# Optimization experiments

Hardware: AMD Instinct MI355X
Metric: run time of the kernel (lower is better)

Reference implementation:

```python
import jax, jax.numpy as jnp
import numpy as np

B, N, E = 8, 4096, 65536
FIN, OUT, T, H = 128, 128, 4, 4
C = OUT // H  # per-head channels
NEG_SLOPE = 0.2
EPS_LN = 1e-5


def setup_inputs() -> dict:
    key = jax.random.key(0)
    ks = jax.random.split(key, 10)
    x = jax.random.normal(ks[0], (B, N, FIN), dtype=jnp.float32)
    edge_index = jax.random.randint(ks[1], (B, 2, E), 0, N, dtype=jnp.int64)
    edge_type = jax.random.randint(ks[2], (B, E), 0, T, dtype=jnp.int64)
    # per-edge-type GATConv params (PyG GATConv: lin weight, att_src, att_dst, bias)
    W = jax.random.normal(ks[3], (T, FIN, H * C), dtype=jnp.float32) / np.sqrt(FIN)
    a_src = jax.random.normal(ks[4], (T, H, C), dtype=jnp.float32) / np.sqrt(C)
    a_dst = jax.random.normal(ks[5], (T, H, C), dtype=jnp.float32) / np.sqrt(C)
    bias = jnp.zeros((T, H * C), dtype=jnp.float32)
    gamma = jnp.ones((OUT,), dtype=jnp.float32)
    beta = jnp.zeros((OUT,), dtype=jnp.float32)
    return {"x": x, "edge_index": edge_index, "edge_type": edge_type,
            "W": W, "a_src": a_src, "a_dst": a_dst, "bias": bias,
            "gamma": gamma, "beta": beta}


def _gat_aggregate(h, src, dst, mask):
    """Single-graph masked GAT aggregation.
    h: [N,H,C] transformed features; src,dst: [E]; mask: [E] bool.
    Returns [N,H,C].
    """
    n = h.shape[0]
    a_s = h[src]                     # [E,H,C] source features (messages)
    # attention logits: att_src . h_src + att_dst . h_dst, done by caller via h-dot
    return a_s, n


def reference(x, edge_index, edge_type, W, a_src, a_dst, bias, gamma, beta):
    b, n, _ = x.shape
    src = edge_index[:, 0, :]  # [B,E]
    dst = edge_index[:, 1, :]

    def per_graph(e_logit, src_b, dst_b, mask_b, h_b):
        # e_logit: [E,H]; h_b: [N,H,C]
        e_m = jnp.where(mask_b[:, None], e_logit, -1e30)
        m = jax.ops.segment_max(e_m, dst_b, num_segments=n)      # [N,H]
        m = jnp.maximum(m, -1e30)
        ex = jnp.exp(e_m - m[dst_b]) * mask_b[:, None]           # [E,H]
        den = jax.ops.segment_sum(ex, dst_b, num_segments=n)     # [N,H]
        alpha = ex / (den[dst_b] + 1e-16)                        # [E,H]
        msg = alpha[:, :, None] * h_b[src_b]                     # [E,H,C]
        return jax.ops.segment_sum(msg, dst_b, num_segments=n)   # [N,H,C]

    out = jnp.zeros((b, n, H * C), dtype=x.dtype)
    for t in range(T):
        h = jnp.einsum('bnf,fo->bno', x, W[t]).reshape(b, n, H, C)
        al_s = jnp.einsum('bnhc,hc->bnh', h, a_src[t])           # [B,N,H]
        al_d = jnp.einsum('bnhc,hc->bnh', h, a_dst[t])
        e = jax.nn.leaky_relu(
            jnp.take_along_axis(al_s, src[..., None], axis=1) +
            jnp.take_along_axis(al_d, dst[..., None], axis=1),
            negative_slope=NEG_SLOPE)                            # [B,E,H]
        mask = (edge_type == t)
        agg = jax.vmap(per_graph)(e, src, dst, mask, h)          # [B,N,H,C]
        out = out + agg.reshape(b, n, H * C) + bias[t]
    # residual + LayerNorm (dropout is identity in eval)
    y = x + out
    mu = jnp.mean(y, axis=-1, keepdims=True)
    var = jnp.var(y, axis=-1, keepdims=True)
    return (y - mu) / jnp.sqrt(var + EPS_LN) * gamma + beta
```

## Files before the change

### kernel.cpp

```cpp
#include <hip/hip_runtime.h>

typedef unsigned int uint;
typedef unsigned short ushort;
typedef __attribute__((ext_vector_type(8))) short short8;
typedef __attribute__((ext_vector_type(4))) float f32x4;

#define Bb 8
#define Nn 4096
#define Ee 65536
#define Tt 4

__device__ __forceinline__ ushort bf16_rne_u(float f) {
    uint u = __float_as_uint(f);
    u += 0x7FFFu + ((u >> 16) & 1u);
    return (ushort)(u >> 16);
}

__global__ __launch_bounds__(256) void prepack_w_kernel(
    const float* __restrict__ W, ushort* __restrict__ Wf)
{
    int gid = blockIdx.x * 256 + threadIdx.x;
    int t    = gid >> 11;
    int rem  = gid & 2047;
    int ks   = rem >> 9;
    int rem2 = rem & 511;
    int nt   = rem2 >> 6;
    int lane = rem2 & 63;
    int n  = nt * 16 + (lane & 15);
    int g  = lane >> 4;
    int k0 = ks * 32 + 4 * g;

    const float* Wt = W + t * 16384;
    union { uint4 q; ushort u[8]; } P;
#pragma unroll
    for (int j = 0; j < 4; ++j) P.u[j]     = bf16_rne_u(Wt[(size_t)(k0 + j) * 128 + n]);
#pragma unroll
    for (int j = 0; j < 4; ++j) P.u[4 + j] = bf16_rne_u(Wt[(size_t)(k0 + 16 + j) * 128 + n]);
    *reinterpret_cast<uint4*>(Wf + (size_t)gid * 8) = P.q;
}

__global__ __launch_bounds__(256, 4) void gemm_mfma_kernel(
    const float* __restrict__ x, const ushort* __restrict__ Wf,
    const float* __restrict__ a_src, const float* __restrict__ a_dst,
    ushort* __restrict__ h, float* __restrict__ al_s, float* __restrict__ al_d)
{
    __shared__ ushort Wlds[16384];
    __shared__ ushort Hst[4096];

    int blk    = blockIdx.x;
    int b      = blk >> 7;
    int rowblk = blk & 127;
    int tid  = threadIdx.x;
    int w    = tid >> 6;
    int lane = tid & 63;
    int nl = lane & 15;
    int g  = lane >> 4;
    int rg  = w & 1;
    int chn = w >> 1;
    int row0 = rowblk * 32 + rg * 16;

    short8 Ah[4], Al[4];
    {
        const float* xr = x + ((size_t)b * Nn + row0 + nl) * 128;
#pragma unroll
        for (int ks = 0; ks < 4; ++ks) {
            float4 fa = *reinterpret_cast<const float4*>(xr + ks * 32 + 4 * g);
            float4 fb = *reinterpret_cast<const float4*>(xr + ks * 32 + 16 + 4 * g);
            float v[8] = {fa.x, fa.y, fa.z, fa.w, fb.x, fb.y, fb.z, fb.w};
            union { short8 s; ushort u[8]; } H, L;
#pragma unroll
            for (int j = 0; j < 8; ++j) {
                ushort hi = bf16_rne_u(v[j]);
                float fh = __uint_as_float(((uint)hi) << 16);
                H.u[j] = hi;
                L.u[j] = bf16_rne_u(v[j] - fh);
            }
            Ah[ks] = H.s;
            Al[ks] = L.s;
        }
    }

    for (int t = 0; t < Tt; ++t) {
        {
            const uint4* src = reinterpret_cast<const uint4*>(Wf + (size_t)t * 16384);
#pragma unroll
            for (int i = 0; i < 8; ++i) {
                uint4 v = src[i * 256 + tid];
                *reinterpret_cast<uint4*>(&Wlds[(i * 256 + tid) * 8]) = v;
            }
        }
        __syncthreads();

        f32x4 acc[4];
#pragma unroll
        for (int i = 0; i < 4; ++i) acc[i] = (f32x4){0.f, 0.f, 0.f, 0.f};
#pragma unroll
        for (int ks = 0; ks < 4; ++ks) {
#pragma unroll
            for (int i = 0; i < 4; ++i) {
                int ntg = chn * 4 + i;
                union { uint4 q; short8 s; } F;
                F.q = *reinterpret_cast<const uint4*>(&Wlds[((ks * 8 + ntg) * 64 + lane) * 8]);
                acc[i] = __builtin_amdgcn_mfma_f32_16x16x32_bf16(Ah[ks], F.s, acc[i], 0, 0, 0);
                acc[i] = __builtin_amdgcn_mfma_f32_16x16x32_bf16(Al[ks], F.s, acc[i], 0, 0, 0);
            }
        }

        {
            float as[4], ad[4];
#pragma unroll
            for (int i = 0; i < 4; ++i) {
                as[i] = a_src[t * 128 + chn * 64 + i * 16 + nl];
                ad[i] = a_dst[t * 128 + chn * 64 + i * 16 + nl];
            }
#pragma unroll
            for (int ih = 0; ih < 2; ++ih) {
#pragma unroll
                for (int r = 0; r < 4; ++r) {
                    float ps = acc[2 * ih][r] * as[2 * ih] + acc[2 * ih + 1][r] * as[2 * ih + 1];
                    float pd = acc[2 * ih][r] * ad[2 * ih] + acc[2 * ih + 1][r] * ad[2 * ih + 1];
#pragma unroll
                    for (int off = 1; off < 16; off <<= 1) {
                        ps += __shfl_xor(ps, off);
                        pd += __shfl_xor(pd, off);
                    }
                    if (nl == 0) {
                        int rowg = row0 + 4 * g + r;
                        int head = 2 * chn + ih;
                        al_s[((size_t)(b * Tt + t) * Nn + rowg) * 4 + head] = ps;
                        al_d[((size_t)(b * Tt + t) * Nn + rowg) * 4 + head] = pd;
                    }
                }
            }
        }

#pragma unroll
        for (int i = 0; i < 4; ++i) {
#pragma unroll
            for (int r = 0; r < 4; ++r) {
                int rowl = rg * 16 + 4 * g + r;
                int col  = chn * 64 + i * 16 + nl;
                uint e = (uint)(rowl * 128) + ((uint)col ^ (uint)(((rowl >> 2) & 3) << 3));
                Hst[e] = bf16_rne_u(acc[i][r]);
            }
        }
        __syncthreads();

        {
            ushort* hb = h + ((size_t)(b * Tt + t) * Nn + (size_t)rowblk * 32) * 128;
#pragma unroll
            for (int it = 0; it < 2; ++it) {
                uint f = (uint)(it * 2048 + tid * 8);
                int rowl = f >> 7;
                uint e = (f & ~127u) + ((f & 127u) ^ (uint)(((rowl >> 2) & 3) << 3));
                uint4 v = *reinterpret_cast<const uint4*>(&Hst[e]);
                *reinterpret_cast<uint4*>(hb + f) = v;
            }
        }
    }
}

__global__ __launch_bounds__(256) void count_kernel(
    const int* __restrict__ ei, const int* __restrict__ et, uint* __restrict__ count)
{
    int i = blockIdx.x * 256 + threadIdx.x;
    int b = i >> 16;
    int e = i & (Ee - 1);
    int dst = ei[(size_t)b * 2 * Ee + Ee + e];
    int t = et[(size_t)b * Ee + e];
    atomicAdd(&count[(((uint)(b * Nn + dst)) << 2) | (uint)t], 1u);
}

__global__ __launch_bounds__(256) void scan1_kernel(
    const uint* __restrict__ cnt, uint* __restrict__ offs, uint* __restrict__ bsum)
{
    __shared__ uint ws[4];
    int tid = threadIdx.x, lane = tid & 63, wv = tid >> 6;
    uint4 c = reinterpret_cast<const uint4*>(cnt)[blockIdx.x * 256 + tid];
    uint tot = c.x + c.y + c.z + c.w;
    uint inc = tot;
#pragma unroll
    for (int d = 1; d < 64; d <<= 1) {
        uint tv = (uint)__shfl_up((int)inc, d);
        if (lane >= d) inc += tv;
    }
    if (lane == 63) ws[wv] = inc;
    __syncthreads();
    uint wexcl = 0;
    for (int w = 0; w < wv; ++w) wexcl += ws[w];
    uint P = wexcl + inc - tot;
    uint4 o;
    o.x = P; o.y = P + c.x; o.z = o.y + c.y; o.w = o.z + c.z;
    reinterpret_cast<uint4*>(offs)[blockIdx.x * 256 + tid] = o;
    if (tid == 255) bsum[blockIdx.x] = P + tot;
}

__global__ __launch_bounds__(128) void scan2_kernel(
    const uint* __restrict__ bsum, uint* __restrict__ bsx)
{
    __shared__ uint w0tot;
    int tid = threadIdx.x, lane = tid & 63, wv = tid >> 6;
    uint v = bsum[tid], inc = v;
#pragma unroll
    for (int d = 1; d < 64; d <<= 1) {
        uint tv = (uint)__shfl_up((int)inc, d);
        if (lane >= d) inc += tv;
    }
    if (tid == 63) w0tot = inc;
    __syncthreads();
    uint add = (wv == 1) ? w0tot : 0u;
    bsx[tid] = add + inc - v;
}

__global__ __launch_bounds__(256) void scatter_lr_kernel(
    const int* __restrict__ ei, const int* __restrict__ et,
    const float* __restrict__ al_s, const float* __restrict__ al_d,
    const uint* __restrict__ offs, const uint* __restrict__ bsx,
    uint* __restrict__ cursor, uint* __restrict__ src_sorted, float4* __restrict__ lr_sorted)
{
    int i = blockIdx.x * 256 + threadIdx.x;
    int b = i >> 16;
    int e = i & (Ee - 1);
    int src = ei[(size_t)b * 2 * Ee + e];
    int dst = ei[(size_t)b * 2 * Ee + Ee + e];
    int t = et[(size_t)b * Ee + e];
    uint g = (((uint)(b * Nn + dst)) << 2) | (uint)t;
    uint slot = atomicAdd(&cursor[g], 1u);
    uint p = offs[g] + bsx[g >> 10] + slot;

    size_t btN = (size_t)(b * Tt + t) * Nn;
    float4 s4 = *reinterpret_cast<const float4*>(&al_s[(btN + src) * 4]);
    float4 d4 = *reinterpret_cast<const float4*>(&al_d[(btN + dst) * 4]);
    float4 lr;
    lr.x = s4.x + d4.x; lr.x = lr.x > 0.f ? lr.x : 0.2f * lr.x;
    lr.y = s4.y + d4.y; lr.y = lr.y > 0.f ? lr.y : 0.2f * lr.y;
    lr.z = s4.z + d4.z; lr.z = lr.z > 0.f ? lr.z : 0.2f * lr.z;
    lr.w = s4.w + d4.w; lr.w = lr.w > 0.f ? lr.w : 0.2f * lr.w;
    src_sorted[p] = (uint)src;
    lr_sorted[p] = lr;
}

__global__ __launch_bounds__(256) void gat_ln_kernel(
    const float* __restrict__ x, const ushort* __restrict__ h,
    const uint* __restrict__ count, const uint* __restrict__ offs, const uint* __restrict__ bsx,
    const uint* __restrict__ src_sorted, const float4* __restrict__ lr_sorted,
    const float* __restrict__ bias, const float* __restrict__ gamma, const float* __restrict__ beta,
    float* __restrict__ out)
{
    __shared__ uint  su_s[4][128];
    __shared__ float ew_s[4][512];
    int wl = threadIdx.x >> 6;
    uint*  su = su_s[wl];
    float* ew = ew_s[wl];

    int wid  = blockIdx.x * 4 + wl;
    int lane = threadIdx.x & 63;
    int b   = wid >> 12;
    int dst = wid & (Nn - 1);
    int eg = lane >> 4;
    int cl = lane & 15;
    int c0 = cl << 3;
    int hh = cl >> 2;

    uint4 cnt4 = reinterpret_cast<const uint4*>(count)[wid];
    uint4 off4 = reinterpret_cast<const uint4*>(offs)[wid];
    uint bsxv  = bsx[((uint)wid) >> 8];
    uint base  = off4.x + bsxv;
    uint D     = min(off4.w + cnt4.w - off4.x, 128u);

    for (uint i = lane; i < D; i += 64) {
        float4 l4 = lr_sorted[base + i];
        su[i] = src_sorted[base + i];
        ew[i * 4 + 0] = __expf(l4.x);
        ew[i * 4 + 1] = __expf(l4.y);
        ew[i * 4 + 2] = __expf(l4.z);
        ew[i * 4 + 3] = __expf(l4.w);
    }

    uint rel[4];
    rel[0] = 0;
    rel[1] = off4.y - off4.x;
    rel[2] = off4.z - off4.x;
    rel[3] = off4.w - off4.x;
    uint ctv[4] = {cnt4.x, cnt4.y, cnt4.z, cnt4.w};

    float tot[8];
#pragma unroll
    for (int k = 0; k < 8; ++k) tot[k] = 0.f;

    for (int t = 0; t < Tt; ++t) {
        uint ct = ctv[t];
        if (!ct) continue;
        uint p0 = rel[t];
        const ushort* hs = h + (size_t)(b * Tt + t) * Nn * 128;

        float acc[8];
#pragma unroll
        for (int k = 0; k < 8; ++k) acc[k] = 0.f;
        float denacc = 0.f;

        for (uint j = 0; j < ct; j += 4) {
            uint jj = j + (uint)eg;
            bool valid = jj < ct;
            uint idx = min(p0 + jj, 127u);
            uint sj = su[idx] & 4095u;
            float aw = valid ? ew[idx * 4 + hh] : 0.f;
            uint4 hv = *reinterpret_cast<const uint4*>(hs + (size_t)sj * 128 + c0);
            float f0 = __uint_as_float(hv.x << 16);
            float f1 = __uint_as_float(hv.x & 0xFFFF0000u);
            float f2 = __uint_as_float(hv.y << 16);
            float f3 = __uint_as_float(hv.y & 0xFFFF0000u);
            float f4 = __uint_as_float(hv.z << 16);
            float f5 = __uint_as_float(hv.z & 0xFFFF0000u);
            float f6 = __uint_as_float(hv.w << 16);
            float f7 = __uint_as_float(hv.w & 0xFFFF0000u);
            acc[0] += aw * f0; acc[1] += aw * f1;
            acc[2] += aw * f2; acc[3] += aw * f3;
            acc[4] += aw * f4; acc[5] += aw * f5;
            acc[6] += aw * f6; acc[7] += aw * f7;
            denacc += aw;
        }
        float d = denacc;
        d += __shfl_xor(d, 1); d += __shfl_xor(d, 2);
        d += __shfl_xor(d, 16); d += __shfl_xor(d, 32);
        float rden = 4.f / (d + 4e-16f);
#pragma unroll
        for (int k = 0; k < 8; ++k) tot[k] += acc[k] * rden;
    }

#pragma unroll
    for (int k = 0; k < 8; ++k) {
        tot[k] += __shfl_xor(tot[k], 16);
        tot[k] += __shfl_xor(tot[k], 32);
    }

    size_t obase = ((size_t)b * Nn + dst) * 128 + c0;
    float y[8];
    {
        float4 xa = *reinterpret_cast<const float4*>(x + obase);
        float4 xb = *reinterpret_cast<const float4*>(x + obase + 4);
        float bs[8];
#pragma unroll
        for (int k = 0; k < 8; ++k) bs[k] = 0.f;
#pragma unroll
        for (int t = 0; t < Tt; ++t) {
            float4 ba = *reinterpret_cast<const float4*>(bias + t * 128 + c0);
            float4 bb = *reinterpret_cast<const float4*>(bias + t * 128 + c0 + 4);
            bs[0] += ba.x; bs[1] += ba.y; bs[2] += ba.z; bs[3] += ba.w;
            bs[4] += bb.x; bs[5] += bb.y; bs[6] += bb.z; bs[7] += bb.w;
        }
        y[0] = xa.x + tot[0] + bs[0]; y[1] = xa.y + tot[1] + bs[1];
        y[2] = xa.z + tot[2] + bs[2]; y[3] = xa.w + tot[3] + bs[3];
        y[4] = xb.x + tot[4] + bs[4]; y[5] = xb.y + tot[5] + bs[5];
        y[6] = xb.z + tot[6] + bs[6]; y[7] = xb.w + tot[7] + bs[7];
    }

    float s = 0.f, ss = 0.f;
#pragma unroll
    for (int k = 0; k < 8; ++k) { s += y[k]; ss += y[k] * y[k]; }
#pragma unroll
    for (int off = 1; off < 16; off <<= 1) {
        s += __shfl_xor(s, off);
        ss += __shfl_xor(ss, off);
    }
    float mu = s * (1.f / 128.f);
    float var = ss * (1.f / 128.f) - mu * mu;
    float rstd = rsqrtf(var + 1e-5f);

    if (eg == 0) {
        float4 ga = *reinterpret_cast<const float4*>(gamma + c0);
        float4 gb = *reinterpret_cast<const float4*>(gamma + c0 + 4);
        float4 ea = *reinterpret_cast<const float4*>(beta + c0);
        float4 eb = *reinterpret_cast<const float4*>(beta + c0 + 4);
        float4 o1, o2;
        o1.x = (y[0] - mu) * rstd * ga.x + ea.x;
        o1.y = (y[1] - mu) * rstd * ga.y + ea.y;
        o1.z = (y[2] - mu) * rstd * ga.z + ea.z;
        o1.w = (y[3] - mu) * rstd * ga.w + ea.w;
        o2.x = (y[4] - mu) * rstd * gb.x + eb.x;
        o2.y = (y[5] - mu) * rstd * gb.y + eb.y;
        o2.z = (y[6] - mu) * rstd * gb.z + eb.z;
        o2.w = (y[7] - mu) * rstd * gb.w + eb.w;
        *reinterpret_cast<float4*>(out + obase) = o1;
        *reinterpret_cast<float4*>(out + obase + 4) = o2;
    }
}

extern "C" void kernel_launch(void* const* d_in, const int* in_sizes, int n_in,
                              void* d_out, int out_size, void* d_ws, size_t ws_size,
                              hipStream_t stream)
{
    const float* x     = (const float*)d_in[0];
    const int*   ei    = (const int*)d_in[1];
    const int*   et    = (const int*)d_in[2];
    const float* W     = (const float*)d_in[3];
    const float* a_src = (const float*)d_in[4];
    const float* a_dst = (const float*)d_in[5];
    const float* bias  = (const float*)d_in[6];
    const float* gamma = (const float*)d_in[7];
    const float* beta  = (const float*)d_in[8];
    float* out = (float*)d_out;

    ushort* h   = (ushort*)d_ws;
    size_t hsz  = (size_t)Bb * Tt * Nn * 128;
    float* al_s = (float*)(h + hsz);
    size_t alsz = (size_t)Bb * Tt * Nn * 4;
    float* al_d = al_s + alsz;
    uint* count  = (uint*)(al_d + alsz);
    uint* cursor = count + (size_t)Bb * Tt * Nn;
    uint* offs   = cursor + (size_t)Bb * Tt * Nn;
    uint* bsum   = offs + (size_t)Bb * Tt * Nn;
    uint* bsx    = bsum + 128;
    uint* src_sorted = bsx + 128;
    float4* lr_sorted = (float4*)(src_sorted + (size_t)Bb * Ee);
    ushort* Wf = (ushort*)(lr_sorted + (size_t)Bb * Ee);

    hipMemsetAsync(count, 0, (size_t)Bb * Tt * Nn * 2 * sizeof(uint), stream);

    prepack_w_kernel<<<32, 256, 0, stream>>>(W, Wf);
    gemm_mfma_kernel<<<Bb * 128, 256, 0, stream>>>(x, Wf, a_src, a_dst, h, al_s, al_d);

    count_kernel<<<(Bb * Ee) / 256, 256, 0, stream>>>(ei, et, count);
    scan1_kernel<<<128, 256, 0, stream>>>(count, offs, bsum);
    scan2_kernel<<<1, 128, 0, stream>>>(bsum, bsx);
    scatter_lr_kernel<<<(Bb * Ee) / 256, 256, 0, stream>>>(
        ei, et, al_s, al_d, offs, bsx, cursor, src_sorted, lr_sorted);

    gat_ln_kernel<<<(Bb * Nn) / 4, 256, 0, stream>>>(
        x, h, count, offs, bsx, src_sorted, lr_sorted, bias, gamma, beta, out);
}
```

Baseline: 206.1 us.

## Fuse preprocessing kernels and remap GAT aggregation to 16-lane groups per node

Merges the count and W-prepack kernels into one launch that also precomputes the summed bias, and folds scan1 into the GEMM launch as extra blocks. The aggregation kernel now handles 16 destination nodes per block, one 16-lane group each, processing edges serially instead of splitting them across four lane groups. This removes the cross-lane shuffle reductions and cuts launch count. The risks are that per-group serial edge loops lengthen the dependency chain on high-degree nodes, and that the per-node edge cache shrinks from 128 to 96 entries.

```diff
diff --git a/kernel.cpp b/kernel.cpp
--- a/kernel.cpp
+++ b/kernel.cpp
@@ -16,41 +16,82 @@
     return (ushort)(u >> 16);
 }
 
-__global__ __launch_bounds__(256) void prepack_w_kernel(
-    const float* __restrict__ W, ushort* __restrict__ Wf)
-{
-    int gid = blockIdx.x * 256 + threadIdx.x;
-    int t    = gid >> 11;
-    int rem  = gid & 2047;
-    int ks   = rem >> 9;
-    int rem2 = rem & 511;
-    int nt   = rem2 >> 6;
-    int lane = rem2 & 63;
-    int n  = nt * 16 + (lane & 15);
-    int g  = lane >> 4;
-    int k0 = ks * 32 + 4 * g;
-
-    const float* Wt = W + t * 16384;
-    union { uint4 q; ushort u[8]; } P;
-#pragma unroll
-    for (int j = 0; j < 4; ++j) P.u[j]     = bf16_rne_u(Wt[(size_t)(k0 + j) * 128 + n]);
-#pragma unroll
-    for (int j = 0; j < 4; ++j) P.u[4 + j] = bf16_rne_u(Wt[(size_t)(k0 + 16 + j) * 128 + n]);
-    *reinterpret_cast<uint4*>(Wf + (size_t)gid * 8) = P.q;
-}
-
-__global__ __launch_bounds__(256, 4) void gemm_mfma_kernel(
+__global__ __launch_bounds__(256) void fused_a_kernel(
+    const int* __restrict__ ei, const int* __restrict__ et, uint* __restrict__ count,
+    const float* __restrict__ W, ushort* __restrict__ Wf,
+    const float* __restrict__ bias, float* __restrict__ bias_sum)
+{
+    int bid = blockIdx.x;
+    int tid = threadIdx.x;
+    if (bid < 2048) {
+        int i = bid * 256 + tid;
+        int b = i >> 16;
+        int e = i & (Ee - 1);
+        int dst = ei[(size_t)b * 2 * Ee + Ee + e];
+        int t = et[(size_t)b * Ee + e];
+        atomicAdd(&count[(((uint)(b * Nn + dst)) << 2) | (uint)t], 1u);
+    } else if (bid < 2080) {
+        int gid = (bid - 2048) * 256 + tid;
+        int t    = gid >> 11;
+        int rem  = gid & 2047;
+        int ks   = rem >> 9;
+        int rem2 = rem & 511;
+        int nt   = rem2 >> 6;
+        int lane = rem2 & 63;
+        int n  = nt * 16 + (lane & 15);
+        int g  = lane >> 4;
+        int k0 = ks * 32 + 4 * g;
+        const float* Wt = W + t * 16384;
+        union { uint4 q; ushort u[8]; } P;
+#pragma unroll
+        for (int j = 0; j < 4; ++j) P.u[j]     = bf16_rne_u(Wt[(size_t)(k0 + j) * 128 + n]);
+#pragma unroll
+        for (int j = 0; j < 4; ++j) P.u[4 + j] = bf16_rne_u(Wt[(size_t)(k0 + 16 + j) * 128 + n]);
+        *reinterpret_cast<uint4*>(Wf + (size_t)gid * 8) = P.q;
+    } else {
+        if (tid < 128)
+            bias_sum[tid] = bias[tid] + bias[128 + tid] + bias[256 + tid] + bias[384 + tid];
+    }
+}
+
+__global__ __launch_bounds__(256, 4) void fused_b_kernel(
     const float* __restrict__ x, const ushort* __restrict__ Wf,
     const float* __restrict__ a_src, const float* __restrict__ a_dst,
-    ushort* __restrict__ h, float* __restrict__ al_s, float* __restrict__ al_d)
+    ushort* __restrict__ h, float* __restrict__ al_s, float* __restrict__ al_d,
+    const uint* __restrict__ cnt, uint* __restrict__ offs, uint* __restrict__ bsum)
 {
     __shared__ ushort Wlds[16384];
     __shared__ ushort Hst[4096];
+
+    int tid = threadIdx.x;
+
+    if (blockIdx.x >= 1024) {
+        uint* ws = reinterpret_cast<uint*>(Hst);
+        int cblk = blockIdx.x - 1024;
+        int lane = tid & 63, wv = tid >> 6;
+        uint4 c = reinterpret_cast<const uint4*>(cnt)[cblk * 256 + tid];
+        uint tot = c.x + c.y + c.z + c.w;
+        uint inc = tot;
+#pragma unroll
+        for (int d = 1; d < 64; d <<= 1) {
+            uint tv = (uint)__shfl_up((int)inc, d);
+            if (lane >= d) inc += tv;
+        }
+        if (lane == 63) ws[wv] = inc;
+        __syncthreads();
+        uint wexcl = 0;
+        for (int w = 0; w < wv; ++w) wexcl += ws[w];
+        uint P = wexcl + inc - tot;
+        uint4 o;
+        o.x = P; o.y = P + c.x; o.z = o.y + c.y; o.w = o.z + c.z;
+        reinterpret_cast<uint4*>(offs)[cblk * 256 + tid] = o;
+        if (tid == 255) bsum[cblk] = P + tot;
+        return;
+    }
 
     int blk    = blockIdx.x;
     int b      = blk >> 7;
     int rowblk = blk & 127;
-    int tid  = threadIdx.x;
     int w    = tid >> 6;
     int lane = tid & 63;
     int nl = lane & 15;
@@ -160,41 +201,6 @@
     }
 }
 
-__global__ __launch_bounds__(256) void count_kernel(
-    const int* __restrict__ ei, const int* __restrict__ et, uint* __restrict__ count)
-{
-    int i = blockIdx.x * 256 + threadIdx.x;
-    int b = i >> 16;
-    int e = i & (Ee - 1);
-    int dst = ei[(size_t)b * 2 * Ee + Ee + e];
-    int t = et[(size_t)b * Ee + e];
-    atomicAdd(&count[(((uint)(b * Nn + dst)) << 2) | (uint)t], 1u);
-}
-
-__global__ __launch_bounds__(256) void scan1_kernel(
-    const uint* __restrict__ cnt, uint* __restrict__ offs, uint* __restrict__ bsum)
-{
-    __shared__ uint ws[4];
-    int tid = threadIdx.x, lane = tid & 63, wv = tid >> 6;
-    uint4 c = reinterpret_cast<const uint4*>(cnt)[blockIdx.x * 256 + tid];
-    uint tot = c.x + c.y + c.z + c.w;
-    uint inc = tot;
-#pragma unroll
-    for (int d = 1; d < 64; d <<= 1) {
-        uint tv = (uint)__shfl_up((int)inc, d);
-        if (lane >= d) inc += tv;
-    }
-    if (lane == 63) ws[wv] = inc;
-    __syncthreads();
-    uint wexcl = 0;
-    for (int w = 0; w < wv; ++w) wexcl += ws[w];
-    uint P = wexcl + inc - tot;
-    uint4 o;
-    o.x = P; o.y = P + c.x; o.z = o.y + c.y; o.w = o.z + c.z;
-    reinterpret_cast<uint4*>(offs)[blockIdx.x * 256 + tid] = o;
-    if (tid == 255) bsum[blockIdx.x] = P + tot;
-}
-
 __global__ __launch_bounds__(128) void scan2_kernel(
     const uint* __restrict__ bsum, uint* __restrict__ bsx)
 {
@@ -244,31 +250,33 @@
     const float* __restrict__ x, const ushort* __restrict__ h,
     const uint* __restrict__ count, const uint* __restrict__ offs, const uint* __restrict__ bsx,
     const uint* __restrict__ src_sorted, const float4* __restrict__ lr_sorted,
-    const float* __restrict__ bias, const float* __restrict__ gamma, const float* __restrict__ beta,
+    const float* __restrict__ bias_sum, const float* __restrict__ gamma, const float* __restrict__ beta,
     float* __restrict__ out)
 {
-    __shared__ uint  su_s[4][128];
-    __shared__ float ew_s[4][512];
-    int wl = threadIdx.x >> 6;
-    uint*  su = su_s[wl];
-    float* ew = ew_s[wl];
-
-    int wid  = blockIdx.x * 4 + wl;
-    int lane = threadIdx.x & 63;
-    int b   = wid >> 12;
-    int dst = wid & (Nn - 1);
-    int eg = lane >> 4;
+    __shared__ uint  su_s[16][96];
+    __shared__ float ew_s[16][96 * 4];
+
+    int tid = threadIdx.x;
+    int wl   = tid >> 6;
+    int lane = tid & 63;
+    int ng = lane >> 4;
     int cl = lane & 15;
     int c0 = cl << 3;
     int hh = cl >> 2;
+    int grp = wl * 4 + ng;
+    uint*  su = su_s[grp];
+    float* ew = ew_s[grp];
+
+    int wid = blockIdx.x * 16 + grp;
+    int b   = wid >> 12;
+    int dst = wid & (Nn - 1);
 
     uint4 cnt4 = reinterpret_cast<const uint4*>(count)[wid];
     uint4 off4 = reinterpret_cast<const uint4*>(offs)[wid];
-    uint bsxv  = bsx[((uint)wid) >> 8];
-    uint base  = off4.x + bsxv;
-    uint D     = min(off4.w + cnt4.w - off4.x, 128u);
-
-    for (uint i = lane; i < D; i += 64) {
+    uint base  = off4.x + bsx[((uint)wid) >> 8];
+    uint D     = min(off4.w + cnt4.w - off4.x, 96u);
+
+    for (uint i = cl; i < D; i += 16) {
         float4 l4 = lr_sorted[base + i];
         su[i] = src_sorted[base + i];
         ew[i * 4 + 0] = __expf(l4.x);
@@ -276,18 +284,16 @@
         ew[i * 4 + 2] = __expf(l4.z);
         ew[i * 4 + 3] = __expf(l4.w);
     }
-
-    uint rel[4];
-    rel[0] = 0;
-    rel[1] = off4.y - off4.x;
-    rel[2] = off4.z - off4.x;
-    rel[3] = off4.w - off4.x;
+    __syncthreads();
+
+    uint rel[4] = {0u, off4.y - off4.x, off4.z - off4.x, off4.w - off4.x};
     uint ctv[4] = {cnt4.x, cnt4.y, cnt4.z, cnt4.w};
 
     float tot[8];
 #pragma unroll
     for (int k = 0; k < 8; ++k) tot[k] = 0.f;
 
+#pragma unroll
     for (int t = 0; t < Tt; ++t) {
         uint ct = ctv[t];
         if (!ct) continue;
@@ -297,14 +303,12 @@
         float acc[8];
 #pragma unroll
         for (int k = 0; k < 8; ++k) acc[k] = 0.f;
-        float denacc = 0.f;
-
-        for (uint j = 0; j < ct; j += 4) {
-            uint jj = j + (uint)eg;
-            bool valid = jj < ct;
-            uint idx = min(p0 + jj, 127u);
-            uint sj = su[idx] & 4095u;
-            float aw = valid ? ew[idx * 4 + hh] : 0.f;
+        float den = 0.f;
+
+        for (uint j = 0; j < ct; ++j) {
+            uint i = p0 + j;
+            float aw = ew[i * 4 + hh];
+            uint  sj = su[i];
             uint4 hv = *reinterpret_cast<const uint4*>(hs + (size_t)sj * 128 + c0);
             float f0 = __uint_as_float(hv.x << 16);
             float f1 = __uint_as_float(hv.x & 0xFFFF0000u);
@@ -318,20 +322,11 @@
             acc[2] += aw * f2; acc[3] += aw * f3;
             acc[4] += aw * f4; acc[5] += aw * f5;
             acc[6] += aw * f6; acc[7] += aw * f7;
-            denacc += aw;
-        }
-        float d = denacc;
-        d += __shfl_xor(d, 1); d += __shfl_xor(d, 2);
-        d += __shfl_xor(d, 16); d += __shfl_xor(d, 32);
-        float rden = 4.f / (d + 4e-16f);
+            den += aw;
+        }
+        float rden = 1.f / (den + 1e-16f);
 #pragma unroll
         for (int k = 0; k < 8; ++k) tot[k] += acc[k] * rden;
-    }
-
-#pragma unroll
-    for (int k = 0; k < 8; ++k) {
-        tot[k] += __shfl_xor(tot[k], 16);
-        tot[k] += __shfl_xor(tot[k], 32);
     }
 
     size_t obase = ((size_t)b * Nn + dst) * 128 + c0;
@@ -339,20 +334,12 @@
     {
         float4 xa = *reinterpret_cast<const float4*>(x + obase);
         float4 xb = *reinterpret_cast<const float4*>(x + obase + 4);
-        float bs[8];
-#pragma unroll
-        for (int k = 0; k < 8; ++k) bs[k] = 0.f;
-#pragma unroll
-        for (int t = 0; t < Tt; ++t) {
-            float4 ba = *reinterpret_cast<const float4*>(bias + t * 128 + c0);
-            float4 bb = *reinterpret_cast<const float4*>(bias + t * 128 + c0 + 4);
-            bs[0] += ba.x; bs[1] += ba.y; bs[2] += ba.z; bs[3] += ba.w;
-            bs[4] += bb.x; bs[5] += bb.y; bs[6] += bb.z; bs[7] += bb.w;
-        }
-        y[0] = xa.x + tot[0] + bs[0]; y[1] = xa.y + tot[1] + bs[1];
-        y[2] = xa.z + tot[2] + bs[2]; y[3] = xa.w + tot[3] + bs[3];
-        y[4] = xb.x + tot[4] + bs[4]; y[5] = xb.y + tot[5] + bs[5];
-        y[6] = xb.z + tot[6] + bs[6]; y[7] = xb.w + tot[7] + bs[7];
+        float4 ba = *reinterpret_cast<const float4*>(bias_sum + c0);
+        float4 bb = *reinterpret_cast<const float4*>(bias_sum + c0 + 4);
+        y[0] = xa.x + tot[0] + ba.x; y[1] = xa.y + tot[1] + ba.y;
+        y[2] = xa.z + tot[2] + ba.z; y[3] = xa.w + tot[3] + ba.w;
+        y[4] = xb.x + tot[4] + bb.x; y[5] = xb.y + tot[5] + bb.y;
+        y[6] = xb.z + tot[6] + bb.z; y[7] = xb.w + tot[7] + bb.w;
     }
 
     float s = 0.f, ss = 0.f;
@@ -367,23 +354,21 @@
     float var = ss * (1.f / 128.f) - mu * mu;
     float rstd = rsqrtf(var + 1e-5f);
 
-    if (eg == 0) {
-        float4 ga = *reinterpret_cast<const float4*>(gamma + c0);
-        float4 gb = *reinterpret_cast<const float4*>(gamma + c0 + 4);
-        float4 ea = *reinterpret_cast<const float4*>(beta + c0);
-        float4 eb = *reinterpret_cast<const float4*>(beta + c0 + 4);
-        float4 o1, o2;
-        o1.x = (y[0] - mu) * rstd * ga.x + ea.x;
-        o1.y = (y[1] - mu) * rstd * ga.y + ea.y;
-        o1.z = (y[2] - mu) * rstd * ga.z + ea.z;
-        o1.w = (y[3] - mu) * rstd * ga.w + ea.w;
-        o2.x = (y[4] - mu) * rstd * gb.x + eb.x;
-        o2.y = (y[5] - mu) * rstd * gb.y + eb.y;
-        o2.z = (y[6] - mu) * rstd * gb.z + eb.z;
-        o2.w = (y[7] - mu) * rstd * gb.w + eb.w;
-        *reinterpret_cast<float4*>(out + obase) = o1;
-        *reinterpret_cast<float4*>(out + obase + 4) = o2;
-    }
+    float4 ga = *reinterpret_cast<const float4*>(gamma + c0);
+    float4 gb = *reinterpret_cast<const float4*>(gamma + c0 + 4);
+    float4 ea = *reinterpret_cast<const float4*>(beta + c0);
+    float4 eb = *reinterpret_cast<const float4*>(beta + c0 + 4);
+    float4 o1, o2;
+    o1.x = (y[0] - mu) * rstd * ga.x + ea.x;
+    o1.y = (y[1] - mu) * rstd * ga.y + ea.y;
+    o1.z = (y[2] - mu) * rstd * ga.z + ea.z;
+    o1.w = (y[3] - mu) * rstd * ga.w + ea.w;
+    o2.x = (y[4] - mu) * rstd * gb.x + eb.x;
+    o2.y = (y[5] - mu) * rstd * gb.y + eb.y;
+    o2.z = (y[6] - mu) * rstd * gb.z + eb.z;
+    o2.w = (y[7] - mu) * rstd * gb.w + eb.w;
+    *reinterpret_cast<float4*>(out + obase) = o1;
+    *reinterpret_cast<float4*>(out + obase + 4) = o2;
 }
 
 extern "C" void kernel_launch(void* const* d_in, const int* in_sizes, int n_in,
@@ -411,21 +396,19 @@
     uint* offs   = cursor + (size_t)Bb * Tt * Nn;
     uint* bsum   = offs + (size_t)Bb * Tt * Nn;
     uint* bsx    = bsum + 128;
-    uint* src_sorted = bsx + 128;
+    float* bias_sum = (float*)(bsx + 128);
+    uint* src_sorted = (uint*)(bias_sum + 128);
     float4* lr_sorted = (float4*)(src_sorted + (size_t)Bb * Ee);
     ushort* Wf = (ushort*)(lr_sorted + (size_t)Bb * Ee);
 
     hipMemsetAsync(count, 0, (size_t)Bb * Tt * Nn * 2 * sizeof(uint), stream);
 
-    prepack_w_kernel<<<32, 256, 0, stream>>>(W, Wf);
-    gemm_mfma_kernel<<<Bb * 128, 256, 0, stream>>>(x, Wf, a_src, a_dst, h, al_s, al_d);
-
-    count_kernel<<<(Bb * Ee) / 256, 256, 0, stream>>>(ei, et, count);
-    scan1_kernel<<<128, 256, 0, stream>>>(count, offs, bsum);
+    fused_a_kernel<<<2081, 256, 0, stream>>>(ei, et, count, W, Wf, bias, bias_sum);
+    fused_b_kernel<<<1152, 256, 0, stream>>>(x, Wf, a_src, a_dst, h, al_s, al_d,
+                                             count, offs, bsum);
     scan2_kernel<<<1, 128, 0, stream>>>(bsum, bsx);
     scatter_lr_kernel<<<(Bb * Ee) / 256, 256, 0, stream>>>(
         ei, et, al_s, al_d, offs, bsx, cursor, src_sorted, lr_sorted);
-
-    gat_ln_kernel<<<(Bb * Nn) / 4, 256, 0, stream>>>(
-        x, h, count, offs, bsx, src_sorted, lr_sorted, bias, gamma, beta, out);
-}
+    gat_ln_kernel<<<(Bb * Nn) / 16, 256, 0, stream>>>(
+        x, h, count, offs, bsx, src_sorted, lr_sorted, bias_sum, gamma, beta, out);
+}
```

New measurement: 186.3 us. 9.6% less time.
